# Kernel tuning notes

Measured on AMD Instinct MI355X. Metric: run time of the kernel, lower is better.

Reference implementation:

```python
import jax, jax.numpy as jnp
import numpy as np

N, E, G, S = 200000, 800000, 2048, 128
NUM_OPS, NUM_ETYPES, NUMERIC = 64, 4, 12
H, TEXT, VOCAB, OUT = 256, 64, 30000, 512
IN0 = 32 + NUMERIC  # 44


def _ln(h, eps=1e-5):
    # nn.LayerNorm with default (ones/zeros) affine, created fresh each forward
    m = h.mean(-1, keepdims=True)
    v = ((h - m) ** 2).mean(-1, keepdims=True)
    return (h - m) * jax.lax.rsqrt(v + eps)


def _leaky(v):
    return jnp.where(v > 0, v, 0.1 * v)  # LeakyReLU(0.1)


def setup_inputs() -> dict:
    key = jax.random.key(0)
    ks = jax.random.split(key, 40)
    x = jax.random.normal(ks[0], (N, 1 + NUMERIC), jnp.float32)
    x = x.at[:, 0].set(jax.random.randint(ks[1], (N,), 0, NUM_OPS).astype(jnp.float32))
    inp = {
        'x': x,
        'edge_index': jax.random.randint(ks[2], (2, E), 0, N),
        'edge_attr': jax.random.randint(ks[3], (E,), 0, NUM_ETYPES),
        'batch': jnp.sort(jax.random.randint(ks[4], (N,), 0, G)),
        'sql_ids': jax.random.randint(ks[5], (G, S), 0, VOCAB),
        'sql_mask': (jax.random.uniform(ks[6], (G, S)) > 0.3).astype(jnp.float32),
        'op_embed': jax.random.normal(ks[7], (NUM_OPS, 32), jnp.float32),
        'edge_embed': jax.random.normal(ks[8], (NUM_ETYPES, 16), jnp.float32),
        'token_embed': jax.random.normal(ks[9], (VOCAB, TEXT), jnp.float32).at[0].set(0.0),  # padding_idx=0
    }
    dims = [IN0, H, H]
    k = 10
    for i, d in enumerate(dims):
        inp[f'lin_w{i}'] = jax.random.normal(ks[k], (d, 16), jnp.float32) * 0.05; k += 1
        inp[f'lin_b{i}'] = jnp.zeros((d,), jnp.float32)
        inp[f'eps{i}'] = jnp.zeros((), jnp.float32)  # train_eps init 0
        inp[f'W1_{i}'] = jax.random.normal(ks[k], (H, d), jnp.float32) * 0.05; k += 1
        inp[f'b1_{i}'] = jnp.zeros((H,), jnp.float32)
        inp[f'W2_{i}'] = jax.random.normal(ks[k], (H, H), jnp.float32) * 0.05; k += 1
        inp[f'b2_{i}'] = jnp.zeros((H,), jnp.float32)
    inp['mW1'] = jax.random.normal(ks[k], (H, H + 3 + TEXT), jnp.float32) * 0.05; k += 1
    inp['mb1'] = jnp.zeros((H,), jnp.float32)
    inp['mW2'] = jax.random.normal(ks[k], (OUT, H), jnp.float32) * 0.05
    inp['mb2'] = jnp.zeros((OUT,), jnp.float32)
    return inp


def reference(x, edge_index, edge_attr, batch, sql_ids, sql_mask,
              op_embed, edge_embed, token_embed,
              lin_w0, lin_b0, eps0, W1_0, b1_0, W2_0, b2_0,
              lin_w1, lin_b1, eps1, W1_1, b1_1, W2_1, b2_1,
              lin_w2, lin_b2, eps2, W1_2, b1_2, W2_2, b2_2,
              mW1, mb1, mW2, mb2):
    op_ids = jnp.clip(x[:, 0].astype(jnp.int32), 0, NUM_OPS - 1)
    nums = x[:, 1:]
    e_idx = jnp.minimum(edge_attr, NUM_ETYPES - 1)  # clamp_max
    edge_emb = edge_embed[e_idx]                    # [E,16]
    h = jnp.concatenate([op_embed[op_ids], nums], 1)  # [N,44]
    src, dst = edge_index[0], edge_index[1]
    convs = [(lin_w0, lin_b0, eps0, W1_0, b1_0, W2_0, b2_0),
             (lin_w1, lin_b1, eps1, W1_1, b1_1, W2_1, b2_1),
             (lin_w2, lin_b2, eps2, W1_2, b1_2, W2_2, b2_2)]
    for (lw, lb, eps, W1, b1, W2, b2) in convs:
        h_in = h
        # GINEConv: msg = relu(x_j + Lin(edge_attr)); sum-aggregate at dst
        msg = jax.nn.relu(h[src] + edge_emb @ lw.T + lb)        # [E,d]
        aggr = jax.ops.segment_sum(msg, dst, num_segments=h.shape[0])
        z = (1.0 + eps) * h + aggr
        h = jax.nn.relu(z @ W1.T + b1) @ W2.T + b2              # conv MLP -> [N,H]
        h = _ln(h)
        h = _leaky(h + h_in) if h_in.shape[-1] == h.shape[-1] else _leaky(h)
    # graph pooling
    g = jax.ops.segment_sum(h, batch, num_segments=G)            # global_add_pool
    count = jax.ops.segment_sum(jnp.ones((h.shape[0],), h.dtype), batch, num_segments=G)
    denom = jnp.maximum(count, 1.0)                              # scatter_mean semantics
    fanout_mean = jax.ops.segment_sum(x[:, 5], batch, num_segments=G) / denom
    cost_mean = jax.ops.segment_sum(x[:, 4], batch, num_segments=G) / denom
    graph_sum = jnp.stack([count, fanout_mean, cost_mean], 1)    # [G,3]
    # text pooling (masked mean)
    emb = token_embed[sql_ids]                                   # [G,S,TEXT]
    summed = (emb * sql_mask[..., None]).sum(1)
    lengths = jnp.maximum(sql_mask.sum(1, keepdims=True), 1.0)
    text_feat = summed / lengths
    cat = jnp.concatenate([g, graph_sum, text_feat], 1)          # [G, H+3+TEXT]
    hid = _leaky(cat @ mW1.T + mb1)                              # Dropout(0.1) is identity in eval
    return hid @ mW2.T + mb2                                     # [G, OUT]
```

## Files before the change

### kernel.cpp

```cpp
#include <hip/hip_runtime.h>

#define NN 200000
#define EE 800000
#define GG 2048
#define NBLK ((NN + 255) / 256)

typedef __attribute__((ext_vector_type(8))) short short8;
typedef __attribute__((ext_vector_type(4))) float f32x4;

__device__ __forceinline__ float bf2f(ushort u){
  unsigned x = ((unsigned)u) << 16;
  return __uint_as_float(x);
}
__device__ __forceinline__ ushort f2bf(float f){
  unsigned x = __float_as_uint(f);
  x += 0x7fffu + ((x >> 16) & 1u);
  return (ushort)(x >> 16);
}

__device__ __forceinline__ void swz256(const float* __restrict__ W, ushort* __restrict__ o, int idx){
  int ks = idx >> 13, rem = idx & 8191;
  int j16 = rem >> 9, rem2 = rem & 511;
  int ln = rem2 >> 3, t = rem2 & 7;
  int row = j16*16 + (ln & 15);
  int k = ks*32 + (ln >> 4)*8 + t;
  o[idx] = f2bf(W[(size_t)row*256 + k]);
}

__global__ __launch_bounds__(256) void prep_k(
    const float* __restrict__ W10, const float* __restrict__ W20,
    const float* __restrict__ W11, const float* __restrict__ W21,
    const float* __restrict__ W12, const float* __restrict__ W22,
    const float* __restrict__ lw0, const float* __restrict__ lb0,
    const float* __restrict__ lw1, const float* __restrict__ lb1,
    const float* __restrict__ lw2, const float* __restrict__ lb2,
    const float* __restrict__ eE, const float* __restrict__ mW1,
    const float* __restrict__ mW2,
    ushort* __restrict__ wb10, ushort* __restrict__ wb20,
    ushort* __restrict__ wb11, ushort* __restrict__ wb21,
    ushort* __restrict__ wb12, ushort* __restrict__ wb22,
    ushort* __restrict__ mW1b, ushort* __restrict__ mW2b,
    float* __restrict__ eb)
{
  int b = blockIdx.x, tid = threadIdx.x;
  if (b < 64){
    int idx = b*256 + tid;
    int ks = idx >> 13, rem = idx & 8191;
    int j16 = rem >> 9, rem2 = rem & 511;
    int ln = rem2 >> 3, t = rem2 & 7;
    int row = j16*16 + (ln & 15);
    int k = ks*32 + (ln >> 4)*8 + t;
    wb10[idx] = (k < 44) ? f2bf(W10[row*44 + k]) : (ushort)0;
    return;
  }
  b -= 64;
  if (b < 256){ swz256(W20, wb20, b*256+tid); return; } b -= 256;
  if (b < 256){ swz256(W11, wb11, b*256+tid); return; } b -= 256;
  if (b < 256){ swz256(W21, wb21, b*256+tid); return; } b -= 256;
  if (b < 256){ swz256(W12, wb12, b*256+tid); return; } b -= 256;
  if (b < 256){ swz256(W22, wb22, b*256+tid); return; } b -= 256;
  if (b < 384){
    int idx = b*256 + tid; int o = idx / 384, k = idx - o*384;
    mW1b[idx] = (k < 323) ? f2bf(mW1[(size_t)o*323 + k]) : (ushort)0;
    return;
  }
  b -= 384;
  if (b < 512){ int idx = b*256+tid; mW2b[idx] = f2bf(mW2[idx]); return; } b -= 512;
  int li = b >> 2, t = b & 3;
  const float* lw = (li == 0) ? lw0 : ((li == 1) ? lw1 : lw2);
  const float* lb = (li == 0) ? lb0 : ((li == 1) ? lb1 : lb2);
  int d = (li == 0) ? 44 : 256;
  float v = 0.f;
  if (tid < d){
    float a = 0.f;
    #pragma unroll
    for (int j = 0; j < 16; j++) a += eE[t*16 + j] * lw[tid*16 + j];
    v = a + lb[tid];
  }
  eb[(li*4 + t)*256 + tid] = v;
}

__global__ __launch_bounds__(256) void build_h0_k(
    const float* __restrict__ x, const float* __restrict__ opE, ushort* __restrict__ h0)
{
  int idx = blockIdx.x*256 + threadIdx.x;
  int i = idx >> 6, c = idx & 63;
  float v = 0.f;
  if (c < 32){
    int op = (int)x[(size_t)i*13];
    op = op < 0 ? 0 : (op > 63 ? 63 : op);
    v = opE[op*32 + c];
  } else if (c < 44){
    v = x[(size_t)i*13 + (c - 31)];
  }
  h0[idx] = f2bf(v);
}

__global__ __launch_bounds__(256) void deg_k(const int* __restrict__ dst, int* __restrict__ D){
  int e = blockIdx.x*256 + threadIdx.x;
  atomicAdd(&D[dst[e]], 1);
}
__global__ __launch_bounds__(256) void scan1_k(int* __restrict__ D, int* __restrict__ bsum){
  __shared__ int s[256];
  int b = blockIdx.x, t = threadIdx.x, idx = b*256 + t;
  int v = (idx < NN) ? D[idx] : 0;
  s[t] = v; __syncthreads();
  for (int off = 1; off < 256; off <<= 1){
    int u = (t >= off) ? s[t-off] : 0;
    __syncthreads();
    s[t] += u;
    __syncthreads();
  }
  if (idx < NN) D[idx] = s[t] - v;
  if (t == 255) bsum[b] = s[255];
}
__global__ __launch_bounds__(256) void scan2_k(int* __restrict__ bsum){
  __shared__ int s[256];
  __shared__ int carry;
  int t = threadIdx.x;
  if (t == 0) carry = 0;
  __syncthreads();
  for (int c0 = 0; c0 < NBLK; c0 += 256){
    int idx = c0 + t;
    int v = (idx < NBLK) ? bsum[idx] : 0;
    s[t] = v; __syncthreads();
    for (int off = 1; off < 256; off <<= 1){
      int u = (t >= off) ? s[t-off] : 0;
      __syncthreads();
      s[t] += u;
      __syncthreads();
    }
    int ex = s[t] - v + carry;
    if (idx < NBLK) bsum[idx] = ex;
    int tot = s[255];
    __syncthreads();
    if (t == 0) carry += tot;
    __syncthreads();
  }
}
__global__ __launch_bounds__(256) void scan3_k(int* __restrict__ D, const int* __restrict__ bsum){
  int b = blockIdx.x, idx = b*256 + threadIdx.x;
  if (idx < NN) D[idx] += bsum[b];
}
__global__ __launch_bounds__(256) void fill_k(const int* __restrict__ src, const int* __restrict__ dst,
                                              const int* __restrict__ et, int* __restrict__ D,
                                              int* __restrict__ csr){
  int e = blockIdx.x*256 + threadIdx.x;
  int d = dst[e];
  int t = et[e]; t = t < 3 ? t : 3;
  int pos = atomicAdd(&D[d], 1);
  csr[pos] = src[e] | (t << 18);
}

template<int KD, int RESID>
__global__ __launch_bounds__(256) void layerf_k(
    const ushort* __restrict__ hsrc, const int* __restrict__ Dend, const int* __restrict__ csr,
    const float* __restrict__ ebL,
    const ushort* __restrict__ W1s, const float* __restrict__ b1,
    const ushort* __restrict__ W2s, const float* __restrict__ b2,
    const float* __restrict__ epsp, ushort* __restrict__ hout)
{
  __shared__ ushort ZT[32][264];
  __shared__ float ebs[1024];
  __shared__ float red1[32][4], red2[32][4], mnL[32], rsL[32];
  const int tid = threadIdx.x, lane = tid & 63, wv = tid >> 6;
  const int l15 = lane & 15, lq = lane >> 4;
  const int rowBase = blockIdx.x * 32;
  const float epv = 1.0f + epsp[0];
  const char* hb = (const char*)hsrc;

  if (KD == 256){
    for (int i = tid; i < 1024; i += 256) ebs[i] = ebL[i];
  } else {
    if (tid < 256) ebs[tid] = ebL[(tid >> 6)*256 + (tid & 63)];
  }
  __syncthreads();

  if (KD == 256){
    int nz; asm("v_mov_b32 %0, 0" : "=v"(nz));
    const int c = lane * 4;
    const unsigned c2 = lane * 8;
    #pragma unroll 1
    for (int it = 0; it < 2; it++){
      int rr0 = wv*8 + it*4;
      int r0 = rowBase + rr0;
      float4 A0, A1, A2, A3;
      {
        ushort4 q0 = *(const ushort4*)(hb + (size_t)(r0+0)*512 + c2);
        ushort4 q1 = *(const ushort4*)(hb + (size_t)(r0+1)*512 + c2);
        ushort4 q2 = *(const ushort4*)(hb + (size_t)(r0+2)*512 + c2);
        ushort4 q3 = *(const ushort4*)(hb + (size_t)(r0+3)*512 + c2);
        A0 = make_float4(epv*bf2f(q0.x), epv*bf2f(q0.y), epv*bf2f(q0.z), epv*bf2f(q0.w));
        A1 = make_float4(epv*bf2f(q1.x), epv*bf2f(q1.y), epv*bf2f(q1.z), epv*bf2f(q1.w));
        A2 = make_float4(epv*bf2f(q2.x), epv*bf2f(q2.y), epv*bf2f(q2.z), epv*bf2f(q2.w));
        A3 = make_float4(epv*bf2f(q3.x), epv*bf2f(q3.y), epv*bf2f(q3.z), epv*bf2f(q3.w));
      }
      int bm1 = (r0 == 0) ? 0 : Dend[r0-1];
      int e0 = Dend[r0], e1 = Dend[r0+1], e2 = Dend[r0+2], e3 = Dend[r0+3];
      int st0 = bm1, st1 = e0, st2 = e1, st3 = e2;
      int n0 = e0 - st0, n1 = e1 - st1, n2 = e2 - st2, n3 = e3 - st3;
      int nmax = n0 > n1 ? n0 : n1;
      nmax = nmax > n2 ? nmax : n2;
      nmax = nmax > n3 ? nmax : n3;
      ushort4 z4; z4.x = z4.y = z4.z = z4.w = 0;
      ushort4 sv0 = z4, sv1 = z4, sv2 = z4, sv3 = z4;
      int t0 = 0, t1 = 0, t2 = 0, t3 = 0;
      int q0 = 0, q1 = 0, q2 = 0, q3 = 0;
      if (n0 > 0){ int p = csr[st0 + nz]; sv0 = *(const ushort4*)(hb + (unsigned)((p & 0x3FFFF) << 9) + c2); t0 = ((p >> 18) & 3)*256; }
      if (n1 > 0){ int p = csr[st1 + nz]; sv1 = *(const ushort4*)(hb + (unsigned)((p & 0x3FFFF) << 9) + c2); t1 = ((p >> 18) & 3)*256; }
      if (n2 > 0){ int p = csr[st2 + nz]; sv2 = *(const ushort4*)(hb + (unsigned)((p & 0x3FFFF) << 9) + c2); t2 = ((p >> 18) & 3)*256; }
      if (n3 > 0){ int p = csr[st3 + nz]; sv3 = *(const ushort4*)(hb + (unsigned)((p & 0x3FFFF) << 9) + c2); t3 = ((p >> 18) & 3)*256; }
      if (n0 > 1) q0 = csr[st0 + 1 + nz];
      if (n1 > 1) q1 = csr[st1 + 1 + nz];
      if (n2 > 1) q2 = csr[st2 + 1 + nz];
      if (n3 > 1) q3 = csr[st3 + 1 + nz];
      for (int k = 0; k < nmax; k++){
        ushort4 c0 = sv0, c1 = sv1, c2v = sv2, c3 = sv3;
        int u0 = t0, u1 = t1, u2 = t2, u3 = t3;
        if (k+1 < n0){ int p = q0; sv0 = *(const ushort4*)(hb + (unsigned)((p & 0x3FFFF) << 9) + c2); t0 = ((p >> 18) & 3)*256; if (k+2 < n0) q0 = csr[st0 + k + 2 + nz]; }
        if (k+1 < n1){ int p = q1; sv1 = *(const ushort4*)(hb + (unsigned)((p & 0x3FFFF) << 9) + c2); t1 = ((p >> 18) & 3)*256; if (k+2 < n1) q1 = csr[st1 + k + 2 + nz]; }
        if (k+1 < n2){ int p = q2; sv2 = *(const ushort4*)(hb + (unsigned)((p & 0x3FFFF) << 9) + c2); t2 = ((p >> 18) & 3)*256; if (k+2 < n2) q2 = csr[st2 + k + 2 + nz]; }
        if (k+1 < n3){ int p = q3; sv3 = *(const ushort4*)(hb + (unsigned)((p & 0x3FFFF) << 9) + c2); t3 = ((p >> 18) & 3)*256; if (k+2 < n3) q3 = csr[st3 + k + 2 + nz]; }
        if (k < n0){
          const float4 ev = *(const float4*)&ebs[u0 + c];
          float v;
          v = bf2f(c0.x) + ev.x; A0.x += v > 0.f ? v : 0.f;
          v = bf2f(c0.y) + ev.y; A0.y += v > 0.f ? v : 0.f;
          v = bf2f(c0.z) + ev.z; A0.z += v > 0.f ? v : 0.f;
          v = bf2f(c0.w) + ev.w; A0.w += v > 0.f ? v : 0.f;
        }
        if (k < n1){
          const float4 ev = *(const float4*)&ebs[u1 + c];
          float v;
          v = bf2f(c1.x) + ev.x; A1.x += v > 0.f ? v : 0.f;
          v = bf2f(c1.y) + ev.y; A1.y += v > 0.f ? v : 0.f;
          v = bf2f(c1.z) + ev.z; A1.z += v > 0.f ? v : 0.f;
          v = bf2f(c1.w) + ev.w; A1.w += v > 0.f ? v : 0.f;
        }
        if (k < n2){
          const float4 ev = *(const float4*)&ebs[u2 + c];
          float v;
          v = bf2f(c2v.x) + ev.x; A2.x += v > 0.f ? v : 0.f;
          v = bf2f(c2v.y) + ev.y; A2.y += v > 0.f ? v : 0.f;
          v = bf2f(c2v.z) + ev.z; A2.z += v > 0.f ? v : 0.f;
          v = bf2f(c2v.w) + ev.w; A2.w += v > 0.f ? v : 0.f;
        }
        if (k < n3){
          const float4 ev = *(const float4*)&ebs[u3 + c];
          float v;
          v = bf2f(c3.x) + ev.x; A3.x += v > 0.f ? v : 0.f;
          v = bf2f(c3.y) + ev.y; A3.y += v > 0.f ? v : 0.f;
          v = bf2f(c3.z) + ev.z; A3.z += v > 0.f ? v : 0.f;
          v = bf2f(c3.w) + ev.w; A3.w += v > 0.f ? v : 0.f;
        }
      }
      ushort4 o;
      o.x = f2bf(A0.x); o.y = f2bf(A0.y); o.z = f2bf(A0.z); o.w = f2bf(A0.w);
      *(ushort4*)&ZT[rr0+0][c] = o;
      o.x = f2bf(A1.x); o.y = f2bf(A1.y); o.z = f2bf(A1.z); o.w = f2bf(A1.w);
      *(ushort4*)&ZT[rr0+1][c] = o;
      o.x = f2bf(A2.x); o.y = f2bf(A2.y); o.z = f2bf(A2.z); o.w = f2bf(A2.w);
      *(ushort4*)&ZT[rr0+2][c] = o;
      o.x = f2bf(A3.x); o.y = f2bf(A3.y); o.z = f2bf(A3.z); o.w = f2bf(A3.w);
      *(ushort4*)&ZT[rr0+3][c] = o;
    }
  } else {
    const int c = l15 * 4;
    const unsigned c2 = l15 * 8;
    const int rrA = wv*8 + lq, rrB = rrA + 4;
    const int rA = rowBase + rrA, rB = rowBase + rrB;
    float aA0, aA1, aA2, aA3, aB0, aB1, aB2, aB3;
    {
      ushort4 hv = *(const ushort4*)(hb + (size_t)rA*128 + c2);
      aA0 = epv*bf2f(hv.x); aA1 = epv*bf2f(hv.y); aA2 = epv*bf2f(hv.z); aA3 = epv*bf2f(hv.w);
      hv = *(const ushort4*)(hb + (size_t)rB*128 + c2);
      aB0 = epv*bf2f(hv.x); aB1 = epv*bf2f(hv.y); aB2 = epv*bf2f(hv.z); aB3 = epv*bf2f(hv.w);
    }
    int stA = (rA == 0) ? 0 : Dend[rA-1], enA = Dend[rA];
    int stB = Dend[rB-1], enB = Dend[rB];
    int nA = enA - stA, nB = enB - stB;
    int nmax = nA > nB ? nA : nB;
    ushort4 svA, svB; int ttA = 0, ttB = 0, pA = 0, pB = 0;
    svA.x = svA.y = svA.z = svA.w = 0; svB = svA;
    if (nA > 0){ int p = csr[stA]; svA = *(const ushort4*)(hb + (unsigned)((p & 0x3FFFF) << 7) + c2); ttA = ((p >> 18) & 3)*64; }
    if (nB > 0){ int p = csr[stB]; svB = *(const ushort4*)(hb + (unsigned)((p & 0x3FFFF) << 7) + c2); ttB = ((p >> 18) & 3)*64; }
    if (nA > 1) pA = csr[stA+1];
    if (nB > 1) pB = csr[stB+1];
    for (int k = 0; k < nmax; k++){
      if (k < nA){
        ushort4 cu = svA;
        const float4 ev = *(const float4*)&ebs[ttA + c];
        if (k+1 < nA){
          int p = pA;
          svA = *(const ushort4*)(hb + (unsigned)((p & 0x3FFFF) << 7) + c2);
          ttA = ((p >> 18) & 3)*64;
          if (k+2 < nA) pA = csr[stA+k+2];
        }
        float v;
        v = bf2f(cu.x) + ev.x; aA0 += v > 0.f ? v : 0.f;
        v = bf2f(cu.y) + ev.y; aA1 += v > 0.f ? v : 0.f;
        v = bf2f(cu.z) + ev.z; aA2 += v > 0.f ? v : 0.f;
        v = bf2f(cu.w) + ev.w; aA3 += v > 0.f ? v : 0.f;
      }
      if (k < nB){
        ushort4 cu = svB;
        const float4 ev = *(const float4*)&ebs[ttB + c];
        if (k+1 < nB){
          int p = pB;
          svB = *(const ushort4*)(hb + (unsigned)((p & 0x3FFFF) << 7) + c2);
          ttB = ((p >> 18) & 3)*64;
          if (k+2 < nB) pB = csr[stB+k+2];
        }
        float v;
        v = bf2f(cu.x) + ev.x; aB0 += v > 0.f ? v : 0.f;
        v = bf2f(cu.y) + ev.y; aB1 += v > 0.f ? v : 0.f;
        v = bf2f(cu.z) + ev.z; aB2 += v > 0.f ? v : 0.f;
        v = bf2f(cu.w) + ev.w; aB3 += v > 0.f ? v : 0.f;
      }
    }
    ushort4 o;
    o.x = f2bf(aA0); o.y = f2bf(aA1); o.z = f2bf(aA2); o.w = f2bf(aA3);
    *(ushort4*)&ZT[rrA][c] = o;
    o.x = f2bf(aB0); o.y = f2bf(aB1); o.z = f2bf(aB2); o.w = f2bf(aB3);
    *(ushort4*)&ZT[rrB][c] = o;
  }
  __syncthreads();

  f32x4 acc[2][4];
  #pragma unroll
  for (int i = 0; i < 2; i++)
    #pragma unroll
    for (int j = 0; j < 4; j++){ f32x4 z = {0.f,0.f,0.f,0.f}; acc[i][j] = z; }

  #pragma unroll
  for (int s = 0; s < KD/32; s++){
    short8 af[2], bfv[4];
    #pragma unroll
    for (int j = 0; j < 4; j++)
      bfv[j] = *(const short8*)(W1s + ((size_t)(s*16 + wv*4 + j)*64 + lane)*8);
    #pragma unroll
    for (int i = 0; i < 2; i++)
      af[i] = *(const short8*)&ZT[i*16 + l15][s*32 + lq*8];
    #pragma unroll
    for (int i = 0; i < 2; i++)
      #pragma unroll
      for (int j = 0; j < 4; j++)
        acc[i][j] = __builtin_amdgcn_mfma_f32_16x16x32_bf16(af[i], bfv[j], acc[i][j], 0, 0, 0);
  }
  __syncthreads();

  {
    float b1c[4];
    #pragma unroll
    for (int j = 0; j < 4; j++) b1c[j] = b1[wv*64 + j*16 + l15];
    #pragma unroll
    for (int i = 0; i < 2; i++)
      #pragma unroll
      for (int j = 0; j < 4; j++){
        int cc = wv*64 + j*16 + l15;
        #pragma unroll
        for (int rg = 0; rg < 4; rg++){
          int r = i*16 + (lq << 2) + rg;
          float v = acc[i][j][rg] + b1c[j];
          v = v > 0.f ? v : 0.f;
          ZT[r][cc] = f2bf(v);
        }
      }
  }
  __syncthreads();

  #pragma unroll
  for (int i = 0; i < 2; i++)
    #pragma unroll
    for (int j = 0; j < 4; j++){ f32x4 z = {0.f,0.f,0.f,0.f}; acc[i][j] = z; }

  #pragma unroll
  for (int s = 0; s < 8; s++){
    short8 af[2], bfv[4];
    #pragma unroll
    for (int j = 0; j < 4; j++)
      bfv[j] = *(const short8*)(W2s + ((size_t)(s*16 + wv*4 + j)*64 + lane)*8);
    #pragma unroll
    for (int i = 0; i < 2; i++)
      af[i] = *(const short8*)&ZT[i*16 + l15][s*32 + lq*8];
    #pragma unroll
    for (int i = 0; i < 2; i++)
      #pragma unroll
      for (int j = 0; j < 4; j++)
        acc[i][j] = __builtin_amdgcn_mfma_f32_16x16x32_bf16(af[i], bfv[j], acc[i][j], 0, 0, 0);
  }

  float b2c[4];
  #pragma unroll
  for (int j = 0; j < 4; j++) b2c[j] = b2[wv*64 + j*16 + l15];
  #pragma unroll
  for (int i = 0; i < 2; i++){
    #pragma unroll
    for (int rg = 0; rg < 4; rg++){
      float s1 = 0.f, s2 = 0.f;
      #pragma unroll
      for (int j = 0; j < 4; j++){
        float y = acc[i][j][rg] + b2c[j];
        s1 += y; s2 += y*y;
      }
      #pragma unroll
      for (int m = 1; m < 16; m <<= 1){
        s1 += __shfl_xor(s1, m, 64);
        s2 += __shfl_xor(s2, m, 64);
      }
      if (l15 == 0){
        int r = i*16 + (lq << 2) + rg;
        red1[r][wv] = s1; red2[r][wv] = s2;
      }
    }
  }
  __syncthreads();
  if (tid < 32){
    float s1 = red1[tid][0] + red1[tid][1] + red1[tid][2] + red1[tid][3];
    float s2 = red2[tid][0] + red2[tid][1] + red2[tid][2] + red2[tid][3];
    float mn = s1 * (1.f/256.f);
    float vr = s2 * (1.f/256.f) - mn*mn;
    mnL[tid] = mn;
    rsL[tid] = rsqrtf(vr + 1e-5f);
  }
  __syncthreads();
  #pragma unroll
  for (int i = 0; i < 2; i++){
    #pragma unroll
    for (int rg = 0; rg < 4; rg++){
      int r = i*16 + (lq << 2) + rg;
      float mn = mnL[r], rs = rsL[r];
      #pragma unroll
      for (int j = 0; j < 4; j++){
        int cc = wv*64 + j*16 + l15;
        float y = acc[i][j][rg] + b2c[j];
        float v = (y - mn) * rs;
        if (!RESID) v = v > 0.f ? v : 0.1f*v;
        ZT[r][cc] = f2bf(v);
      }
    }
  }
  __syncthreads();
  #pragma unroll
  for (int p = 0; p < 8; p++){
    int r = p*4 + (tid >> 6);
    int cs = (tid & 63) * 4;
    ushort4 zt = *(const ushort4*)&ZT[r][cs];
    ushort4 o;
    if (RESID){
      ushort4 rv = *(const ushort4*)(hsrc + (size_t)(rowBase + r)*256 + cs);
      float v0 = bf2f(zt.x) + bf2f(rv.x);
      float v1 = bf2f(zt.y) + bf2f(rv.y);
      float v2 = bf2f(zt.z) + bf2f(rv.z);
      float v3 = bf2f(zt.w) + bf2f(rv.w);
      o.x = f2bf(v0 > 0.f ? v0 : 0.1f*v0);
      o.y = f2bf(v1 > 0.f ? v1 : 0.1f*v1);
      o.z = f2bf(v2 > 0.f ? v2 : 0.1f*v2);
      o.w = f2bf(v3 > 0.f ? v3 : 0.1f*v3);
    } else {
      o = zt;
    }
    *(ushort4*)(hout + (size_t)(rowBase + r)*256 + cs) = o;
  }
}

__global__ __launch_bounds__(256) void readout_k(
    const ushort* __restrict__ h, const int* __restrict__ batch, const float* __restrict__ x,
    const int* __restrict__ sqlIds, const float* __restrict__ sqlMask,
    const float* __restrict__ tok, ushort* __restrict__ catb)
{
  int g = blockIdx.x, tid = threadIdx.x;
  const int lane = tid & 63, wv = tid >> 6;
  __shared__ int se[2];
  __shared__ float part[4][256];
  __shared__ float tpart[4][64];
  __shared__ float mpart[4];
  __shared__ float xs[2];
  if (tid < 2){
    int target = g + tid;
    int lo = 0, hi = NN;
    while (lo < hi){ int mid = (lo + hi) >> 1; if (batch[mid] < target) lo = mid + 1; else hi = mid; }
    se[tid] = lo;
  }
  __syncthreads();
  int start = se[0], end = se[1];
  {
    float a0 = 0.f, a1 = 0.f, a2 = 0.f, a3 = 0.f;
    for (int i = start + wv; i < end; i += 4){
      ushort4 q = *(const ushort4*)(h + (size_t)i*256 + lane*4);
      a0 += bf2f(q.x); a1 += bf2f(q.y); a2 += bf2f(q.z); a3 += bf2f(q.w);
    }
    part[wv][lane*4 + 0] = a0;
    part[wv][lane*4 + 1] = a1;
    part[wv][lane*4 + 2] = a2;
    part[wv][lane*4 + 3] = a3;
  }
  if (wv >= 2){
    int col = (wv == 2) ? 5 : 4;
    float s = 0.f;
    for (int i = start + lane; i < end; i += 64) s += x[(size_t)i*13 + col];
    #pragma unroll
    for (int m = 1; m < 64; m <<= 1) s += __shfl_xor(s, m, 64);
    if (lane == 0) xs[wv - 2] = s;
  }
  {
    int c = lane;
    float acc = 0.f, m = 0.f;
    for (int s = wv; s < 128; s += 4){
      int id = sqlIds[g*128 + s];
      float mk = sqlMask[g*128 + s];
      m += mk;
      acc += tok[(size_t)id*64 + c] * mk;
    }
    tpart[wv][c] = acc;
    if (c == 0) mpart[wv] = m;
  }
  __syncthreads();
  {
    float gsum = part[0][tid] + part[1][tid] + part[2][tid] + part[3][tid];
    catb[(size_t)g*384 + tid] = f2bf(gsum);
  }
  if (tid == 0){
    float cnt = (float)(end - start);
    float dn = cnt > 1.f ? cnt : 1.f;
    catb[(size_t)g*384 + 256] = f2bf(cnt);
    catb[(size_t)g*384 + 257] = f2bf(xs[0] / dn);
    catb[(size_t)g*384 + 258] = f2bf(xs[1] / dn);
  }
  if (tid < 64){
    float L = mpart[0] + mpart[1] + mpart[2] + mpart[3];
    L = L > 1.f ? L : 1.f;
    float tsum = tpart[0][tid] + tpart[1][tid] + tpart[2][tid] + tpart[3][tid];
    catb[(size_t)g*384 + 259 + tid] = f2bf(tsum / L);
  }
  if (tid >= 64 && tid < 125){
    catb[(size_t)g*384 + 259 + tid] = 0;
  }
}

__global__ __launch_bounds__(256) void head1_k(
    const ushort* __restrict__ catb, const ushort* __restrict__ W1b,
    const float* __restrict__ b1, ushort* __restrict__ hidb)
{
  __shared__ ushort smem[64*72 + 256*72];
  ushort (*As)[72] = (ushort(*)[72])smem;
  ushort (*Ws)[72] = (ushort(*)[72])(smem + 64*72);
  const int tid = threadIdx.x, lane = tid & 63, wv = tid >> 6;
  const int rowBase = blockIdx.x * 64;
  f32x4 acc[4][4];
  #pragma unroll
  for (int i = 0; i < 4; i++)
    #pragma unroll
    for (int j = 0; j < 4; j++){ f32x4 z = {0.f,0.f,0.f,0.f}; acc[i][j] = z; }

  for (int k0 = 0; k0 < 384; k0 += 64){
    __syncthreads();
    #pragma unroll
    for (int p = 0; p < 4; p++){
      int r = p*16 + (tid >> 4);
      int kk = (tid & 15) * 4;
      *(ushort4*)&As[r][kk] = *(const ushort4*)(catb + (size_t)(rowBase + r)*384 + k0 + kk);
    }
    #pragma unroll
    for (int p = 0; p < 16; p++){
      int oc = p*16 + (tid >> 4);
      int kk = (tid & 15) * 4;
      *(ushort4*)&Ws[oc][kk] = *(const ushort4*)(W1b + (size_t)oc*384 + k0 + kk);
    }
    __syncthreads();
    #pragma unroll
    for (int kc = 0; kc < 2; kc++){
      short8 af[4], bfv[4];
      #pragma unroll
      for (int i = 0; i < 4; i++)
        af[i] = *(const short8*)&As[i*16 + (lane & 15)][kc*32 + (lane >> 4)*8];
      #pragma unroll
      for (int j = 0; j < 4; j++)
        bfv[j] = *(const short8*)&Ws[wv*64 + j*16 + (lane & 15)][kc*32 + (lane >> 4)*8];
      #pragma unroll
      for (int i = 0; i < 4; i++)
        #pragma unroll
        for (int j = 0; j < 4; j++)
          acc[i][j] = __builtin_amdgcn_mfma_f32_16x16x32_bf16(af[i], bfv[j], acc[i][j], 0, 0, 0);
    }
  }
  __syncthreads();
  ushort (*Cs)[264] = (ushort(*)[264])smem;
  #pragma unroll
  for (int j = 0; j < 4; j++){
    int cc = wv*64 + j*16 + (lane & 15);
    float bb = b1[cc];
    #pragma unroll
    for (int i = 0; i < 4; i++){
      #pragma unroll
      for (int rg = 0; rg < 4; rg++){
        int r = i*16 + ((lane >> 4) << 2) + rg;
        float v = acc[i][j][rg] + bb;
        v = v > 0.f ? v : 0.1f*v;
        Cs[r][cc] = f2bf(v);
      }
    }
  }
  __syncthreads();
  #pragma unroll
  for (int p = 0; p < 16; p++){
    int r = p*4 + (tid >> 6);
    int c = (tid & 63) * 4;
    *(ushort4*)(hidb + (size_t)(rowBase + r)*256 + c) = *(const ushort4*)&Cs[r][c];
  }
}

__global__ __launch_bounds__(256) void head2_k(
    const ushort* __restrict__ hidb, const ushort* __restrict__ W2b,
    const float* __restrict__ b2, float* __restrict__ out)
{
  __shared__ float smemf[128*132];
  ushort (*As)[72] = (ushort(*)[72])smemf;
  ushort (*Bs)[72] = (ushort(*)[72])((ushort*)smemf + 128*72);
  const int tid = threadIdx.x, lane = tid & 63, wv = tid >> 6;
  const int wr = (wv >> 1) * 64;
  const int wc = (wv & 1) * 64;
  const int rowBase = blockIdx.x * 128;
  const int colBase = blockIdx.y * 128;
  const int lr = tid >> 4, lk = (tid & 15) * 4;

  f32x4 acc[4][4];
  #pragma unroll
  for (int i = 0; i < 4; i++)
    #pragma unroll
    for (int j = 0; j < 4; j++){ f32x4 z = {0.f,0.f,0.f,0.f}; acc[i][j] = z; }

  for (int k0 = 0; k0 < 256; k0 += 64){
    __syncthreads();
    #pragma unroll
    for (int p = 0; p < 8; p++){
      int r = lr + p*16;
      *(ushort4*)&As[r][lk] = *(const ushort4*)(hidb + (size_t)(rowBase + r)*256 + k0 + lk);
      *(ushort4*)&Bs[r][lk] = *(const ushort4*)(W2b + (size_t)(colBase + r)*256 + k0 + lk);
    }
    __syncthreads();
    #pragma unroll
    for (int kc = 0; kc < 2; kc++){
      short8 af[4], bfv[4];
      #pragma unroll
      for (int i = 0; i < 4; i++)
        af[i] = *(const short8*)&As[wr + i*16 + (lane & 15)][kc*32 + (lane >> 4)*8];
      #pragma unroll
      for (int j = 0; j < 4; j++)
        bfv[j] = *(const short8*)&Bs[wc + j*16 + (lane & 15)][kc*32 + (lane >> 4)*8];
      #pragma unroll
      for (int i = 0; i < 4; i++)
        #pragma unroll
        for (int j = 0; j < 4; j++)
          acc[i][j] = __builtin_amdgcn_mfma_f32_16x16x32_bf16(af[i], bfv[j], acc[i][j], 0, 0, 0);
    }
  }
  __syncthreads();
  float (*Cs)[132] = (float(*)[132])smemf;
  #pragma unroll
  for (int j = 0; j < 4; j++){
    int cl = wc + j*16 + (lane & 15);
    float bb = b2[colBase + cl];
    #pragma unroll
    for (int i = 0; i < 4; i++){
      int r0 = wr + i*16 + ((lane >> 4) << 2);
      #pragma unroll
      for (int rg = 0; rg < 4; rg++)
        Cs[r0 + rg][cl] = acc[i][j][rg] + bb;
    }
  }
  __syncthreads();
  #pragma unroll
  for (int p = 0; p < 16; p++){
    int r = (tid >> 5) + p*8;
    int c4 = (tid & 31) * 4;
    *(float4*)(out + (size_t)(rowBase + r)*512 + colBase + c4) = *(const float4*)&Cs[r][c4];
  }
}

extern "C" void kernel_launch(void* const* d_in, const int* in_sizes, int n_in,
                              void* d_out, int out_size, void* d_ws, size_t ws_size,
                              hipStream_t stream)
{
  const float* x       = (const float*)d_in[0];
  const int*   ei      = (const int*)d_in[1];
  const int*   src     = ei;
  const int*   dst     = ei + EE;
  const int*   eattr   = (const int*)d_in[2];
  const int*   batch   = (const int*)d_in[3];
  const int*   sqlIds  = (const int*)d_in[4];
  const float* sqlMask = (const float*)d_in[5];
  const float* opE     = (const float*)d_in[6];
  const float* eE      = (const float*)d_in[7];
  const float* tok     = (const float*)d_in[8];
  const float* lw0 = (const float*)d_in[9],  *lb0 = (const float*)d_in[10], *eps0 = (const float*)d_in[11];
  const float* W10 = (const float*)d_in[12], *b10 = (const float*)d_in[13];
  const float* W20 = (const float*)d_in[14], *b20 = (const float*)d_in[15];
  const float* lw1 = (const float*)d_in[16], *lb1 = (const float*)d_in[17], *eps1 = (const float*)d_in[18];
  const float* W11 = (const float*)d_in[19], *b11 = (const float*)d_in[20];
  const float* W21 = (const float*)d_in[21], *b21 = (const float*)d_in[22];
  const float* lw2 = (const float*)d_in[23], *lb2 = (const float*)d_in[24], *eps2 = (const float*)d_in[25];
  const float* W12 = (const float*)d_in[26], *b12 = (const float*)d_in[27];
  const float* W22 = (const float*)d_in[28], *b22 = (const float*)d_in[29];
  const float* mW1 = (const float*)d_in[30], *mb1 = (const float*)d_in[31];
  const float* mW2 = (const float*)d_in[32], *mb2 = (const float*)d_in[33];
  float* out = (float*)d_out;

  char* ws = (char*)d_ws;
  size_t off = 0;
  const size_t NB256 = (size_t)NN*256*2;
  ushort* bufH    = (ushort*)(ws + off); off += NB256;
  char*   region  = ws + off;            off += NB256;
  ushort* h0      = (ushort*)region;
  ushort* hPong   = (ushort*)region;
  ushort* catb    = (ushort*)region;
  ushort* hidb    = (ushort*)(region + (size_t)GG*384*2);
  ushort* wb10 = (ushort*)(ws + off); off += (size_t)256*64*2;
  ushort* wb20 = (ushort*)(ws + off); off += (size_t)65536*2;
  ushort* wb11 = (ushort*)(ws + off); off += (size_t)65536*2;
  ushort* wb21 = (ushort*)(ws + off); off += (size_t)65536*2;
  ushort* wb12 = (ushort*)(ws + off); off += (size_t)65536*2;
  ushort* wb22 = (ushort*)(ws + off); off += (size_t)65536*2;
  ushort* mW1b = (ushort*)(ws + off); off += (size_t)256*384*2;
  ushort* mW2b = (ushort*)(ws + off); off += (size_t)512*256*2;
  float*  eb   = (float*)(ws + off);  off += (size_t)3*4*256*4;
  int* D    = (int*)(ws + off); off += (size_t)NN*4;
  int* bsum = (int*)(ws + off); off += (size_t)NBLK*4;
  int* csr  = (int*)(ws + off); off += (size_t)EE*4;
  size_t needFast = off;

  if (ws_size < needFast) return;

  prep_k<<<2252, 256, 0, stream>>>(W10, W20, W11, W21, W12, W22,
                                   lw0, lb0, lw1, lb1, lw2, lb2, eE, mW1, mW2,
                                   wb10, wb20, wb11, wb21, wb12, wb22, mW1b, mW2b, eb);
  build_h0_k<<<50000, 256, 0, stream>>>(x, opE, h0);

  hipMemsetAsync(D, 0, (size_t)NN*4, stream);
  deg_k<<<3125, 256, 0, stream>>>(dst, D);
  scan1_k<<<NBLK, 256, 0, stream>>>(D, bsum);
  scan2_k<<<1, 256, 0, stream>>>(bsum);
  scan3_k<<<NBLK, 256, 0, stream>>>(D, bsum);
  fill_k<<<3125, 256, 0, stream>>>(src, dst, eattr, D, csr);

  layerf_k<64,0><<<6250, 256, 0, stream>>>(h0,    D, csr, eb,        wb10, b10, wb20, b20, eps0, bufH);
  layerf_k<256,1><<<6250, 256, 0, stream>>>(bufH, D, csr, eb + 1024, wb11, b11, wb21, b21, eps1, hPong);
  layerf_k<256,1><<<6250, 256, 0, stream>>>(hPong,D, csr, eb + 2048, wb12, b12, wb22, b22, eps2, bufH);

  readout_k<<<GG, 256, 0, stream>>>(bufH, batch, x, sqlIds, sqlMask, tok, catb);
  head1_k<<<32, 256, 0, stream>>>(catb, mW1b, mb1, hidb);
  head2_k<<<dim3(16, 4), 256, 0, stream>>>(hidb, mW2b, mb2, out);
}
```

Measured before the change: 831.2 us.

## Double layer kernel row tile to 64 rows with 512-thread blocks

The fused GIN layer kernel now processes 64 node rows per block with 8 waves instead of 32 rows with 4 waves. Each wave computes a 64x32 output slice rather than 32x64, so each weight fragment loaded from global memory is reused across four row tiles instead of two, halving weight traffic per row. Shared memory for reductions and the edge-embedding table is merged into one aux buffer to make room for the larger ZT tile. The risks are fewer resident blocks per CU because of the larger LDS and register footprint, and more waves waiting at each block-wide barrier.

```diff
diff --git a/kernel.cpp b/kernel.cpp
--- a/kernel.cpp
+++ b/kernel.cpp
@@ -153,26 +153,29 @@
 }
 
 template<int KD, int RESID>
-__global__ __launch_bounds__(256) void layerf_k(
+__global__ __launch_bounds__(512) void layerf_k(
     const ushort* __restrict__ hsrc, const int* __restrict__ Dend, const int* __restrict__ csr,
     const float* __restrict__ ebL,
     const ushort* __restrict__ W1s, const float* __restrict__ b1,
     const ushort* __restrict__ W2s, const float* __restrict__ b2,
     const float* __restrict__ epsp, ushort* __restrict__ hout)
 {
-  __shared__ ushort ZT[32][264];
-  __shared__ float ebs[1024];
-  __shared__ float red1[32][4], red2[32][4], mnL[32], rsL[32];
+  __shared__ ushort ZT[64][264];
+  __shared__ float aux[1152];
+  float* red1 = aux;
+  float* red2 = aux + 512;
+  float* mnL  = aux + 1024;
+  float* rsL  = aux + 1088;
   const int tid = threadIdx.x, lane = tid & 63, wv = tid >> 6;
   const int l15 = lane & 15, lq = lane >> 4;
-  const int rowBase = blockIdx.x * 32;
+  const int rowBase = blockIdx.x * 64;
   const float epv = 1.0f + epsp[0];
   const char* hb = (const char*)hsrc;
 
   if (KD == 256){
-    for (int i = tid; i < 1024; i += 256) ebs[i] = ebL[i];
+    for (int i = tid; i < 1024; i += 512) aux[i] = ebL[i];
   } else {
-    if (tid < 256) ebs[tid] = ebL[(tid >> 6)*256 + (tid & 63)];
+    if (tid < 256) aux[tid] = ebL[(tid >> 6)*256 + (tid & 63)];
   }
   __syncthreads();
 
@@ -222,7 +225,7 @@
         if (k+1 < n2){ int p = q2; sv2 = *(const ushort4*)(hb + (unsigned)((p & 0x3FFFF) << 9) + c2); t2 = ((p >> 18) & 3)*256; if (k+2 < n2) q2 = csr[st2 + k + 2 + nz]; }
         if (k+1 < n3){ int p = q3; sv3 = *(const ushort4*)(hb + (unsigned)((p & 0x3FFFF) << 9) + c2); t3 = ((p >> 18) & 3)*256; if (k+2 < n3) q3 = csr[st3 + k + 2 + nz]; }
         if (k < n0){
-          const float4 ev = *(const float4*)&ebs[u0 + c];
+          const float4 ev = *(const float4*)&aux[u0 + c];
           float v;
           v = bf2f(c0.x) + ev.x; A0.x += v > 0.f ? v : 0.f;
           v = bf2f(c0.y) + ev.y; A0.y += v > 0.f ? v : 0.f;
@@ -230,7 +233,7 @@
           v = bf2f(c0.w) + ev.w; A0.w += v > 0.f ? v : 0.f;
         }
         if (k < n1){
-          const float4 ev = *(const float4*)&ebs[u1 + c];
+          const float4 ev = *(const float4*)&aux[u1 + c];
           float v;
           v = bf2f(c1.x) + ev.x; A1.x += v > 0.f ? v : 0.f;
           v = bf2f(c1.y) + ev.y; A1.y += v > 0.f ? v : 0.f;
@@ -238,7 +241,7 @@
           v = bf2f(c1.w) + ev.w; A1.w += v > 0.f ? v : 0.f;
         }
         if (k < n2){
-          const float4 ev = *(const float4*)&ebs[u2 + c];
+          const float4 ev = *(const float4*)&aux[u2 + c];
           float v;
           v = bf2f(c2v.x) + ev.x; A2.x += v > 0.f ? v : 0.f;
           v = bf2f(c2v.y) + ev.y; A2.y += v > 0.f ? v : 0.f;
@@ -246,7 +249,7 @@
           v = bf2f(c2v.w) + ev.w; A2.w += v > 0.f ? v : 0.f;
         }
         if (k < n3){
-          const float4 ev = *(const float4*)&ebs[u3 + c];
+          const float4 ev = *(const float4*)&aux[u3 + c];
           float v;
           v = bf2f(c3.x) + ev.x; A3.x += v > 0.f ? v : 0.f;
           v = bf2f(c3.y) + ev.y; A3.y += v > 0.f ? v : 0.f;
@@ -289,7 +292,7 @@
     for (int k = 0; k < nmax; k++){
       if (k < nA){
         ushort4 cu = svA;
-        const float4 ev = *(const float4*)&ebs[ttA + c];
+        const float4 ev = *(const float4*)&aux[ttA + c];
         if (k+1 < nA){
           int p = pA;
           svA = *(const ushort4*)(hb + (unsigned)((p & 0x3FFFF) << 7) + c2);
@@ -304,7 +307,7 @@
       }
       if (k < nB){
         ushort4 cu = svB;
-        const float4 ev = *(const float4*)&ebs[ttB + c];
+        const float4 ev = *(const float4*)&aux[ttB + c];
         if (k+1 < nB){
           int p = pB;
           svB = *(const ushort4*)(hb + (unsigned)((p & 0x3FFFF) << 7) + c2);
@@ -326,38 +329,38 @@
   }
   __syncthreads();
 
-  f32x4 acc[2][4];
-  #pragma unroll
-  for (int i = 0; i < 2; i++)
-    #pragma unroll
-    for (int j = 0; j < 4; j++){ f32x4 z = {0.f,0.f,0.f,0.f}; acc[i][j] = z; }
+  f32x4 acc[4][2];
+  #pragma unroll
+  for (int i = 0; i < 4; i++)
+    #pragma unroll
+    for (int j = 0; j < 2; j++){ f32x4 z = {0.f,0.f,0.f,0.f}; acc[i][j] = z; }
 
   #pragma unroll
   for (int s = 0; s < KD/32; s++){
-    short8 af[2], bfv[4];
-    #pragma unroll
-    for (int j = 0; j < 4; j++)
-      bfv[j] = *(const short8*)(W1s + ((size_t)(s*16 + wv*4 + j)*64 + lane)*8);
-    #pragma unroll
-    for (int i = 0; i < 2; i++)
+    short8 af[4], bfv[2];
+    #pragma unroll
+    for (int j = 0; j < 2; j++)
+      bfv[j] = *(const short8*)(W1s + ((size_t)(s*16 + wv*2 + j)*64 + lane)*8);
+    #pragma unroll
+    for (int i = 0; i < 4; i++)
       af[i] = *(const short8*)&ZT[i*16 + l15][s*32 + lq*8];
     #pragma unroll
-    for (int i = 0; i < 2; i++)
-      #pragma unroll
-      for (int j = 0; j < 4; j++)
+    for (int i = 0; i < 4; i++)
+      #pragma unroll
+      for (int j = 0; j < 2; j++)
         acc[i][j] = __builtin_amdgcn_mfma_f32_16x16x32_bf16(af[i], bfv[j], acc[i][j], 0, 0, 0);
   }
   __syncthreads();
 
   {
-    float b1c[4];
-    #pragma unroll
-    for (int j = 0; j < 4; j++) b1c[j] = b1[wv*64 + j*16 + l15];
-    #pragma unroll
-    for (int i = 0; i < 2; i++)
-      #pragma unroll
-      for (int j = 0; j < 4; j++){
-        int cc = wv*64 + j*16 + l15;
+    float b1c[2];
+    #pragma unroll
+    for (int j = 0; j < 2; j++) b1c[j] = b1[wv*32 + j*16 + l15];
+    #pragma unroll
+    for (int i = 0; i < 4; i++)
+      #pragma unroll
+      for (int j = 0; j < 2; j++){
+        int cc = wv*32 + j*16 + l15;
         #pragma unroll
         for (int rg = 0; rg < 4; rg++){
           int r = i*16 + (lq << 2) + rg;
@@ -370,36 +373,36 @@
   __syncthreads();
 
   #pragma unroll
-  for (int i = 0; i < 2; i++)
-    #pragma unroll
-    for (int j = 0; j < 4; j++){ f32x4 z = {0.f,0.f,0.f,0.f}; acc[i][j] = z; }
+  for (int i = 0; i < 4; i++)
+    #pragma unroll
+    for (int j = 0; j < 2; j++){ f32x4 z = {0.f,0.f,0.f,0.f}; acc[i][j] = z; }
 
   #pragma unroll
   for (int s = 0; s < 8; s++){
-    short8 af[2], bfv[4];
-    #pragma unroll
-    for (int j = 0; j < 4; j++)
-      bfv[j] = *(const short8*)(W2s + ((size_t)(s*16 + wv*4 + j)*64 + lane)*8);
-    #pragma unroll
-    for (int i = 0; i < 2; i++)
+    short8 af[4], bfv[2];
+    #pragma unroll
+    for (int j = 0; j < 2; j++)
+      bfv[j] = *(const short8*)(W2s + ((size_t)(s*16 + wv*2 + j)*64 + lane)*8);
+    #pragma unroll
+    for (int i = 0; i < 4; i++)
       af[i] = *(const short8*)&ZT[i*16 + l15][s*32 + lq*8];
     #pragma unroll
-    for (int i = 0; i < 2; i++)
-      #pragma unroll
-      for (int j = 0; j < 4; j++)
+    for (int i = 0; i < 4; i++)
+      #pragma unroll
+      for (int j = 0; j < 2; j++)
         acc[i][j] = __builtin_amdgcn_mfma_f32_16x16x32_bf16(af[i], bfv[j], acc[i][j], 0, 0, 0);
   }
 
-  float b2c[4];
-  #pragma unroll
-  for (int j = 0; j < 4; j++) b2c[j] = b2[wv*64 + j*16 + l15];
-  #pragma unroll
-  for (int i = 0; i < 2; i++){
+  float b2c[2];
+  #pragma unroll
+  for (int j = 0; j < 2; j++) b2c[j] = b2[wv*32 + j*16 + l15];
+  #pragma unroll
+  for (int i = 0; i < 4; i++){
     #pragma unroll
     for (int rg = 0; rg < 4; rg++){
       float s1 = 0.f, s2 = 0.f;
       #pragma unroll
-      for (int j = 0; j < 4; j++){
+      for (int j = 0; j < 2; j++){
         float y = acc[i][j][rg] + b2c[j];
         s1 += y; s2 += y*y;
       }
@@ -410,14 +413,15 @@
       }
       if (l15 == 0){
         int r = i*16 + (lq << 2) + rg;
-        red1[r][wv] = s1; red2[r][wv] = s2;
-      }
-    }
-  }
-  __syncthreads();
-  if (tid < 32){
-    float s1 = red1[tid][0] + red1[tid][1] + red1[tid][2] + red1[tid][3];
-    float s2 = red2[tid][0] + red2[tid][1] + red2[tid][2] + red2[tid][3];
+        red1[r*8 + wv] = s1; red2[r*8 + wv] = s2;
+      }
+    }
+  }
+  __syncthreads();
+  if (tid < 64){
+    float s1 = 0.f, s2 = 0.f;
+    #pragma unroll
+    for (int w = 0; w < 8; w++){ s1 += red1[tid*8 + w]; s2 += red2[tid*8 + w]; }
     float mn = s1 * (1.f/256.f);
     float vr = s2 * (1.f/256.f) - mn*mn;
     mnL[tid] = mn;
@@ -425,14 +429,14 @@
   }
   __syncthreads();
   #pragma unroll
-  for (int i = 0; i < 2; i++){
+  for (int i = 0; i < 4; i++){
     #pragma unroll
     for (int rg = 0; rg < 4; rg++){
       int r = i*16 + (lq << 2) + rg;
       float mn = mnL[r], rs = rsL[r];
       #pragma unroll
-      for (int j = 0; j < 4; j++){
-        int cc = wv*64 + j*16 + l15;
+      for (int j = 0; j < 2; j++){
+        int cc = wv*32 + j*16 + l15;
         float y = acc[i][j][rg] + b2c[j];
         float v = (y - mn) * rs;
         if (!RESID) v = v > 0.f ? v : 0.1f*v;
@@ -443,7 +447,7 @@
   __syncthreads();
   #pragma unroll
   for (int p = 0; p < 8; p++){
-    int r = p*4 + (tid >> 6);
+    int r = p*8 + (tid >> 6);
     int cs = (tid & 63) * 4;
     ushort4 zt = *(const ushort4*)&ZT[r][cs];
     ushort4 o;
@@ -743,9 +747,9 @@
   scan3_k<<<NBLK, 256, 0, stream>>>(D, bsum);
   fill_k<<<3125, 256, 0, stream>>>(src, dst, eattr, D, csr);
 
-  layerf_k<64,0><<<6250, 256, 0, stream>>>(h0,    D, csr, eb,        wb10, b10, wb20, b20, eps0, bufH);
-  layerf_k<256,1><<<6250, 256, 0, stream>>>(bufH, D, csr, eb + 1024, wb11, b11, wb21, b21, eps1, hPong);
-  layerf_k<256,1><<<6250, 256, 0, stream>>>(hPong,D, csr, eb + 2048, wb12, b12, wb22, b22, eps2, bufH);
+  layerf_k<64,0><<<3125, 512, 0, stream>>>(h0,    D, csr, eb,        wb10, b10, wb20, b20, eps0, bufH);
+  layerf_k<256,1><<<3125, 512, 0, stream>>>(bufH, D, csr, eb + 1024, wb11, b11, wb21, b21, eps1, hPong);
+  layerf_k<256,1><<<3125, 512, 0, stream>>>(hPong,D, csr, eb + 2048, wb12, b12, wb22, b22, eps2, bufH);
 
   readout_k<<<GG, 256, 0, stream>>>(bufH, batch, x, sqlIds, sqlMask, tok, catb);
   head1_k<<<32, 256, 0, stream>>>(catb, mW1b, mb1, hidb);
```

Result: slower. 909.6 us (+9.4%).
